# Performance work log

Measured on AMD Instinct MI355X. Metric: run time of the kernel, lower is better.

Reference implementation:

```python
import jax, jax.numpy as jnp
import numpy as np

N = 100000
E = 1600000
F_IN = 512
HEADS = 8
C1 = 8          # per-head channels layer 1
C2 = 16         # num_classes, layer 2 (heads=1)
NEG_SLOPE = 0.2


def gat_conv(x, W, att_src, att_dst, bias, edge_index, heads, ch):
    """PyG-style GATConv (eval mode, add_self_loops=True, concat).
    x: [N, Fin], W: [Fin, heads*ch], att_*: [heads, ch], bias: [heads*ch]."""
    n = x.shape[0]
    loop = jnp.arange(n, dtype=edge_index.dtype)
    src = jnp.concatenate([edge_index[0], loop])   # [E+N]
    dst = jnp.concatenate([edge_index[1], loop])

    h = (x @ W).reshape(n, heads, ch)                       # [N, H, C]
    a_src = jnp.einsum('nhc,hc->nh', h, att_src)            # [N, H]
    a_dst = jnp.einsum('nhc,hc->nh', h, att_dst)

    e = a_src[src] + a_dst[dst]                             # [E+N, H]
    e = jax.nn.leaky_relu(e, NEG_SLOPE)
    # segment softmax over destination nodes
    m = jax.ops.segment_max(e, dst, num_segments=n)         # [N, H]
    ex = jnp.exp(e - m[dst])
    denom = jax.ops.segment_sum(ex, dst, num_segments=n)    # [N, H]
    alpha = ex / (denom[dst] + 1e-16)                       # [E+N, H]

    msg = h[src] * alpha[..., None]                         # [E+N, H, C]
    out = jax.ops.segment_sum(msg, dst, num_segments=n)     # [N, H, C]
    return out.reshape(n, heads * ch) + bias


def setup_inputs() -> dict:
    key = jax.random.key(0)
    ks = jax.random.split(key, 10)
    glorot = lambda k, shape: jax.random.normal(k, shape, jnp.float32) * np.sqrt(2.0 / (shape[0] + shape[-1]))
    return {
        'x': jax.random.normal(ks[0], (N, F_IN), jnp.float32),
        'edge_index': jax.random.randint(ks[1], (2, E), 0, N, jnp.int64),
        'W1': glorot(ks[2], (F_IN, HEADS * C1)),
        'att_src1': glorot(ks[3], (HEADS, C1)),
        'att_dst1': glorot(ks[4], (HEADS, C1)),
        'b1': jnp.zeros((HEADS * C1,), jnp.float32),
        'W2': glorot(ks[5], (HEADS * C1, C2)),
        'att_src2': glorot(ks[6], (1, C2)),
        'att_dst2': glorot(ks[7], (1, C2)),
        'b2': jnp.zeros((C2,), jnp.float32),
    }


def reference(x, edge_index, W1, att_src1, att_dst1, b1, W2, att_src2, att_dst2, b2):
    # eval mode: all F.dropout / internal attention dropout are identity
    h = gat_conv(x, W1, att_src1, att_dst1, b1, edge_index, HEADS, C1)   # [N, 64]
    h = jax.nn.elu(h)
    h = gat_conv(h, W2, att_src2, att_dst2, b2, edge_index, 1, C2)       # [N, C2]
    return jax.nn.log_softmax(h, axis=1)
```

## Files before the change

### kernel.cpp

```cpp
#include <hip/hip_runtime.h>
#include <hip/hip_bf16.h>

#define NEG_SLOPE 0.2f

typedef __attribute__((ext_vector_type(8))) short  bf16x8;
typedef __attribute__((ext_vector_type(8))) unsigned short u16x8;
typedef __attribute__((ext_vector_type(4))) unsigned short u16x4;
typedef __attribute__((ext_vector_type(4))) float  f32x4;

static __device__ __forceinline__ ushort f2bf(float f) {
    union { float f; unsigned int u; } c; c.f = f;
    unsigned int r = c.u + 0x7fffu + ((c.u >> 16) & 1u);
    return (ushort)(r >> 16);
}
static __device__ __forceinline__ float bf2f(ushort u) {
    union { unsigned int u; float f; } c; c.u = ((unsigned int)u) << 16;
    return c.f;
}

__global__ __launch_bounds__(256) void gemm1_mfma(
    const float* __restrict__ x, const float* __restrict__ W,
    const float* __restrict__ att_src, const float* __restrict__ att_dst,
    ushort* __restrict__ h1b, float* __restrict__ asrc, float* __restrict__ adst, int n)
{
    __shared__ ushort Bs[64][520];
    const int t    = threadIdx.x;
    const int lane = t & 63;
    const int wv   = t >> 6;
    const int rb   = blockIdx.x * 64;
    const int m    = lane & 15;
    const int kg   = lane >> 4;

    #pragma unroll 4
    for (int i = 0; i < 32; ++i) {
        int idx = (t + i * 256) * 4;
        float4 v = *(const float4*)(W + idx);
        int k = idx >> 6, c = idx & 63;
        Bs[c + 0][k] = f2bf(v.x); Bs[c + 1][k] = f2bf(v.y);
        Bs[c + 2][k] = f2bf(v.z); Bs[c + 3][k] = f2bf(v.w);
    }

    const int arow  = rb + wv * 16 + m;
    const int arowc = min(arow, n - 1);
    const float* xp = x + (size_t)arowc * 512 + kg * 8;

    f32x4 acc[4] = {};
    __syncthreads();

    #pragma unroll 8
    for (int k32 = 0; k32 < 16; ++k32) {
        float4 lo = *(const float4*)(xp + k32 * 32);
        float4 hi = *(const float4*)(xp + k32 * 32 + 4);
        u16x8 a;
        a[0] = f2bf(lo.x); a[1] = f2bf(lo.y); a[2] = f2bf(lo.z); a[3] = f2bf(lo.w);
        a[4] = f2bf(hi.x); a[5] = f2bf(hi.y); a[6] = f2bf(hi.z); a[7] = f2bf(hi.w);
        bf16x8 af = *(bf16x8*)&a;
        #pragma unroll
        for (int t4 = 0; t4 < 4; ++t4) {
            bf16x8 bfr = *(const bf16x8*)&Bs[t4 * 16 + m][k32 * 32 + kg * 8];
            acc[t4] = __builtin_amdgcn_mfma_f32_16x16x32_bf16(af, bfr, acc[t4], 0, 0, 0);
        }
    }

    #pragma unroll
    for (int t4 = 0; t4 < 4; ++t4) {
        const float as_w = att_src[t4 * 16 + m];
        const float ad_w = att_dst[t4 * 16 + m];
        #pragma unroll
        for (int i = 0; i < 4; ++i) {
            int gr = rb + wv * 16 + kg * 4 + i;
            float v = acc[t4][i];
            float ps = v * as_w, pd = v * ad_w;
            ps += __shfl_xor(ps, 1); pd += __shfl_xor(pd, 1);
            ps += __shfl_xor(ps, 2); pd += __shfl_xor(pd, 2);
            ps += __shfl_xor(ps, 4); pd += __shfl_xor(pd, 4);
            if (gr < n) {
                h1b[(size_t)gr * 64 + t4 * 16 + m] = f2bf(v);
                if ((m & 7) == 0) {
                    int h = t4 * 2 + (m >> 3);
                    asrc[gr * 8 + h] = ps;
                    adst[gr * 8 + h] = pd;
                }
            }
        }
    }
}

__global__ __launch_bounds__(256) void hist_k(
    const int* __restrict__ ei, int* __restrict__ cnt, int* __restrict__ slot, int E)
{
    int t = blockIdx.x * blockDim.x + threadIdx.x;
    if (t < E) slot[t] = atomicAdd(&cnt[ei[E + t]], 1);
}

#define SCAN_B 256
#define SCAN_T 256

__global__ __launch_bounds__(SCAN_T) void scan_a(const int* __restrict__ cnt, int* __restrict__ bsum, int n)
{
    __shared__ int sh[SCAN_T];
    const int tid = threadIdx.x;
    const int per = (n + SCAN_B * SCAN_T - 1) / (SCAN_B * SCAN_T);
    const int lo = (blockIdx.x * SCAN_T + tid) * per;
    const int hi = min(n, lo + per);
    int s = 0;
    for (int i = lo; i < hi; ++i) s += cnt[i];
    sh[tid] = s;
    __syncthreads();
    #pragma unroll
    for (int o = SCAN_T / 2; o; o >>= 1) {
        if (tid < o) sh[tid] += sh[tid + o];
        __syncthreads();
    }
    if (tid == 0) bsum[blockIdx.x] = sh[0];
}

__global__ __launch_bounds__(SCAN_T) void scan_b(
    const int* __restrict__ cnt, const int* __restrict__ bsum,
    int* __restrict__ rowptr, int n, int E)
{
    __shared__ int sb[SCAN_B];
    __shared__ int sh[SCAN_T];
    const int tid = threadIdx.x;
    sb[tid] = bsum[tid];
    __syncthreads();
    #pragma unroll
    for (int o = 1; o < SCAN_B; o <<= 1) {
        int v = (tid >= o) ? sb[tid - o] : 0;
        __syncthreads();
        sb[tid] += v;
        __syncthreads();
    }
    const int boff = (blockIdx.x == 0) ? 0 : sb[blockIdx.x - 1];

    const int per = (n + SCAN_B * SCAN_T - 1) / (SCAN_B * SCAN_T);
    const int lo = (blockIdx.x * SCAN_T + tid) * per;
    const int hi = min(n, lo + per);
    int s = 0;
    for (int i = lo; i < hi; ++i) s += cnt[i];
    sh[tid] = s;
    __syncthreads();
    #pragma unroll
    for (int o = 1; o < SCAN_T; o <<= 1) {
        int v = (tid >= o) ? sh[tid - o] : 0;
        __syncthreads();
        sh[tid] += v;
        __syncthreads();
    }
    int excl = boff + ((tid == 0) ? 0 : sh[tid - 1]);
    for (int i = lo; i < hi; ++i) { rowptr[i] = excl; excl += cnt[i]; }
    if (blockIdx.x == 0 && tid == 0) rowptr[n] = E;
}

__global__ __launch_bounds__(256) void scatter_k(
    const int* __restrict__ ei, const int* __restrict__ rowptr,
    const int* __restrict__ slot, int* __restrict__ ssrc, int E)
{
    int t = blockIdx.x * blockDim.x + threadIdx.x;
    if (t >= E) return;
    int d = ei[E + t];
    ssrc[rowptr[d] + slot[t]] = ei[t];
}

__global__ __launch_bounds__(256) void agg1_k(
    const int* __restrict__ rowptr, const int* __restrict__ ssrc,
    const float* __restrict__ asrc1, const float* __restrict__ adst1,
    const ushort* __restrict__ h1b, const float* __restrict__ b1,
    const float* __restrict__ W2, const float* __restrict__ att_src2, const float* __restrict__ att_dst2,
    ushort* __restrict__ h2b, float* __restrict__ asrc2, float* __restrict__ adst2, int n)
{
    __shared__ float Ws2[64 * 17];
    __shared__ float sv[4][64];
    const int t = threadIdx.x;
    #pragma unroll
    for (int k = 0; k < 4; ++k) {
        int idx = t + k * 256;
        Ws2[(idx >> 4) * 17 + (idx & 15)] = W2[idx];
    }
    __syncthreads();

    const int wv = t >> 6;
    const int j  = t & 63;
    const int g  = j >> 3;
    const int h  = j & 7;
    const int node = blockIdx.x * 4 + wv;
    const bool active = node < n;

    if (active) {
        const int d = node;
        const int start = rowptr[d], end = rowptr[d + 1];
        const float adsth = adst1[d * 8 + h];
        float acc0[8] = {}, acc1[8] = {};
        float dsum0 = 0.f, dsum1 = 0.f;
        for (int base = start - 1; base < end; base += 16) {
            int i0 = base + g;
            int i1 = i0 + 8;
            if (i0 < end) {
                int s = (i0 < start) ? d : ssrc[i0];
                float e = asrc1[s * 8 + h] + adsth;
                e = e > 0.f ? e : NEG_SLOPE * e;
                float ex = __expf(e);
                dsum0 += ex;
                u16x8 hv = *(const u16x8*)(h1b + (size_t)s * 64 + h * 8);
                #pragma unroll
                for (int c = 0; c < 8; ++c) acc0[c] += ex * bf2f(hv[c]);
            }
            if (i1 < end) {
                int s = ssrc[i1];
                float e = asrc1[s * 8 + h] + adsth;
                e = e > 0.f ? e : NEG_SLOPE * e;
                float ex = __expf(e);
                dsum1 += ex;
                u16x8 hv = *(const u16x8*)(h1b + (size_t)s * 64 + h * 8);
                #pragma unroll
                for (int c = 0; c < 8; ++c) acc1[c] += ex * bf2f(hv[c]);
            }
        }
        float dsum = dsum0 + dsum1;
        float acc[8];
        #pragma unroll
        for (int c = 0; c < 8; ++c) acc[c] = acc0[c] + acc1[c];
        #pragma unroll
        for (int o = 8; o < 64; o <<= 1) {
            dsum += __shfl_xor(dsum, o);
            #pragma unroll
            for (int c = 0; c < 8; ++c) acc[c] += __shfl_xor(acc[c], o);
        }
        if (g == 0) {
            float den = dsum + 1e-16f;
            #pragma unroll
            for (int c = 0; c < 8; ++c) {
                float v = acc[c] / den + b1[h * 8 + c];
                v = v > 0.f ? v : (__expf(v) - 1.f);
                sv[wv][h * 8 + c] = v;
            }
        }
    }
    __syncthreads();

    if (active) {
        const int c = j & 15, q = j >> 4;
        float p = 0.f;
        #pragma unroll
        for (int r = 0; r < 16; ++r)
            p += sv[wv][q * 16 + r] * Ws2[(q * 16 + r) * 17 + c];
        p += __shfl_xor(p, 16);
        p += __shfl_xor(p, 32);
        if (j < 16) h2b[(size_t)node * 16 + j] = f2bf(p);
        float as2 = p * att_src2[c];
        float ad2 = p * att_dst2[c];
        #pragma unroll
        for (int o = 1; o < 16; o <<= 1) { as2 += __shfl_xor(as2, o, 16); ad2 += __shfl_xor(ad2, o, 16); }
        if (j == 0) { asrc2[node] = as2; adst2[node] = ad2; }
    }
}

__global__ __launch_bounds__(256) void agg2_k(
    const int* __restrict__ rowptr, const int* __restrict__ ssrc,
    const float* __restrict__ asrc2, const float* __restrict__ adst2,
    const ushort* __restrict__ h2b, const float* __restrict__ b2,
    float* __restrict__ out, int n)
{
    const int t = threadIdx.x;
    const int node = blockIdx.x * 4 + (t >> 6);
    if (node >= n) return;
    const int j = t & 63;
    const int g = j >> 2;
    const int q = j & 3;
    const int d = node;
    const int start = rowptr[d], end = rowptr[d + 1];
    const float adst_d = adst2[d];

    float acc0[4] = {}, acc1[4] = {};
    float dsum0 = 0.f, dsum1 = 0.f;
    for (int base = start - 1; base < end; base += 32) {
        int i0 = base + g;
        int i1 = i0 + 16;
        if (i0 < end) {
            int s = (i0 < start) ? d : ssrc[i0];
            float e = asrc2[s] + adst_d;
            e = e > 0.f ? e : NEG_SLOPE * e;
            float ex = __expf(e);
            dsum0 += ex;
            u16x4 hv = *(const u16x4*)(h2b + (size_t)s * 16 + q * 4);
            #pragma unroll
            for (int c = 0; c < 4; ++c) acc0[c] += ex * bf2f(hv[c]);
        }
        if (i1 < end) {
            int s = ssrc[i1];
            float e = asrc2[s] + adst_d;
            e = e > 0.f ? e : NEG_SLOPE * e;
            float ex = __expf(e);
            dsum1 += ex;
            u16x4 hv = *(const u16x4*)(h2b + (size_t)s * 16 + q * 4);
            #pragma unroll
            for (int c = 0; c < 4; ++c) acc1[c] += ex * bf2f(hv[c]);
        }
    }
    float dsum = dsum0 + dsum1;
    float acc[4];
    #pragma unroll
    for (int c = 0; c < 4; ++c) acc[c] = acc0[c] + acc1[c];
    #pragma unroll
    for (int o = 4; o < 64; o <<= 1) {
        dsum += __shfl_xor(dsum, o);
        #pragma unroll
        for (int c = 0; c < 4; ++c) acc[c] += __shfl_xor(acc[c], o);
    }

    const float den = dsum + 1e-16f;
    float v[4];
    float m = -1e30f;
    #pragma unroll
    for (int c = 0; c < 4; ++c) {
        v[c] = acc[c] / den + b2[q * 4 + c];
        m = fmaxf(m, v[c]);
    }
    m = fmaxf(m, __shfl_xor(m, 1));
    m = fmaxf(m, __shfl_xor(m, 2));
    float s2 = 0.f;
    #pragma unroll
    for (int c = 0; c < 4; ++c) s2 += __expf(v[c] - m);
    s2 += __shfl_xor(s2, 1);
    s2 += __shfl_xor(s2, 2);
    const float lse = m + logf(s2);
    if (j < 4) {
        float4 o4 = make_float4(v[0] - lse, v[1] - lse, v[2] - lse, v[3] - lse);
        *(float4*)(out + (size_t)d * 16 + q * 4) = o4;
    }
}

extern "C" void kernel_launch(void* const* d_in, const int* in_sizes, int n_in,
                              void* d_out, int out_size, void* d_ws, size_t ws_size,
                              hipStream_t stream) {
    const float* x        = (const float*)d_in[0];
    const int*   ei       = (const int*)d_in[1];
    const float* W1       = (const float*)d_in[2];
    const float* att_src1 = (const float*)d_in[3];
    const float* att_dst1 = (const float*)d_in[4];
    const float* b1       = (const float*)d_in[5];
    const float* W2       = (const float*)d_in[6];
    const float* att_src2 = (const float*)d_in[7];
    const float* att_dst2 = (const float*)d_in[8];
    const float* b2       = (const float*)d_in[9];
    float* out = (float*)d_out;

    const int n = in_sizes[0] / 512;
    const int E = in_sizes[1] / 2;

    char* base = (char*)d_ws;
    ushort* h1b   = (ushort*)(base);
    ushort* h2b   = (ushort*)(base + (size_t)128 * n);
    float*  asrc1 = (float*) (base + (size_t)160 * n);
    float*  adst1 = (float*) (base + (size_t)192 * n);
    float*  asrc2 = (float*) (base + (size_t)224 * n);
    float*  adst2 = (float*) (base + (size_t)228 * n);
    int*    rowptr= (int*)   (base + (size_t)232 * n);
    int*    cnt   = (int*)   (base + (size_t)236 * n + 4);
    int*    bsum  = (int*)   (base + (size_t)240 * n + 4);
    int*    slot  = (int*)   (base + (size_t)240 * n + 4 + 1024);
    int*    ssrc  = slot + E;

    hipMemsetAsync(cnt, 0, (size_t)4 * n, stream);

    hist_k<<<(E + 255) / 256, 256, 0, stream>>>(ei, cnt, slot, E);
    scan_a<<<SCAN_B, SCAN_T, 0, stream>>>(cnt, bsum, n);
    scan_b<<<SCAN_B, SCAN_T, 0, stream>>>(cnt, bsum, rowptr, n, E);
    scatter_k<<<(E + 255) / 256, 256, 0, stream>>>(ei, rowptr, slot, ssrc, E);

    gemm1_mfma<<<(n + 63) / 64, 256, 0, stream>>>(x, W1, att_src1, att_dst1, h1b, asrc1, adst1, n);

    agg1_k<<<(n + 3) / 4, 256, 0, stream>>>(rowptr, ssrc, asrc1, adst1, h1b, b1,
                                            W2, att_src2, att_dst2, h2b, asrc2, adst2, n);

    agg2_k<<<(n + 3) / 4, 256, 0, stream>>>(rowptr, ssrc, asrc2, adst2, h2b, b2, out, n);
}
```

Before: 300.2 us.

## Pre-transpose W1 to bf16, double-buffer x loads, and use 128-row gemm1 blocks

A new small kernel converts W1 to a transposed bf16 copy once per call, so each gemm1 block loads B into shared memory with plain vector copies instead of per-block conversion and scattered stores. gemm1 now uses 512 threads covering 128 rows, which halves how many times each block loads W. The x row loads are prefetched two k-steps ahead to hide global-memory latency behind the MFMAs. The trade-off is an extra launch, plus higher register use and lower occupancy from the larger blocks. The workspace layout is also recomputed with aligned offsets.

```diff
diff --git a/kernel.cpp b/kernel.cpp
--- a/kernel.cpp
+++ b/kernel.cpp
@@ -18,8 +18,16 @@
     return c.f;
 }
 
-__global__ __launch_bounds__(256) void gemm1_mfma(
-    const float* __restrict__ x, const float* __restrict__ W,
+__global__ __launch_bounds__(256) void prep_w1(const float* __restrict__ W, ushort* __restrict__ W1T)
+{
+    int idx = blockIdx.x * 256 + threadIdx.x;
+    if (idx >= 64 * 512) return;
+    int c = idx >> 9, k = idx & 511;
+    W1T[idx] = f2bf(W[k * 64 + c]);
+}
+
+__global__ __launch_bounds__(512, 4) void gemm1_mfma(
+    const float* __restrict__ x, const ushort* __restrict__ W1T,
     const float* __restrict__ att_src, const float* __restrict__ att_dst,
     ushort* __restrict__ h1b, float* __restrict__ asrc, float* __restrict__ adst, int n)
 {
@@ -27,17 +35,16 @@
     const int t    = threadIdx.x;
     const int lane = t & 63;
     const int wv   = t >> 6;
-    const int rb   = blockIdx.x * 64;
+    const int rb   = blockIdx.x * 128;
     const int m    = lane & 15;
     const int kg   = lane >> 4;
 
-    #pragma unroll 4
-    for (int i = 0; i < 32; ++i) {
-        int idx = (t + i * 256) * 4;
-        float4 v = *(const float4*)(W + idx);
-        int k = idx >> 6, c = idx & 63;
-        Bs[c + 0][k] = f2bf(v.x); Bs[c + 1][k] = f2bf(v.y);
-        Bs[c + 2][k] = f2bf(v.z); Bs[c + 3][k] = f2bf(v.w);
+    #pragma unroll
+    for (int i = 0; i < 8; ++i) {
+        int chunk = t + i * 512;
+        int c  = chunk >> 6;
+        int ko = (chunk & 63) * 8;
+        *(u16x8*)&Bs[c][ko] = *(const u16x8*)(W1T + c * 512 + ko);
     }
 
     const int arow  = rb + wv * 16 + m;
@@ -47,19 +54,27 @@
     f32x4 acc[4] = {};
     __syncthreads();
 
-    #pragma unroll 8
+    float4 lo0 = *(const float4*)(xp);
+    float4 hi0 = *(const float4*)(xp + 4);
+    float4 lo1 = *(const float4*)(xp + 32);
+    float4 hi1 = *(const float4*)(xp + 36);
+    #pragma unroll
     for (int k32 = 0; k32 < 16; ++k32) {
-        float4 lo = *(const float4*)(xp + k32 * 32);
-        float4 hi = *(const float4*)(xp + k32 * 32 + 4);
+        float4 nlo = {}, nhi = {};
+        if (k32 < 14) {
+            nlo = *(const float4*)(xp + (k32 + 2) * 32);
+            nhi = *(const float4*)(xp + (k32 + 2) * 32 + 4);
+        }
         u16x8 a;
-        a[0] = f2bf(lo.x); a[1] = f2bf(lo.y); a[2] = f2bf(lo.z); a[3] = f2bf(lo.w);
-        a[4] = f2bf(hi.x); a[5] = f2bf(hi.y); a[6] = f2bf(hi.z); a[7] = f2bf(hi.w);
+        a[0] = f2bf(lo0.x); a[1] = f2bf(lo0.y); a[2] = f2bf(lo0.z); a[3] = f2bf(lo0.w);
+        a[4] = f2bf(hi0.x); a[5] = f2bf(hi0.y); a[6] = f2bf(hi0.z); a[7] = f2bf(hi0.w);
         bf16x8 af = *(bf16x8*)&a;
         #pragma unroll
         for (int t4 = 0; t4 < 4; ++t4) {
             bf16x8 bfr = *(const bf16x8*)&Bs[t4 * 16 + m][k32 * 32 + kg * 8];
             acc[t4] = __builtin_amdgcn_mfma_f32_16x16x32_bf16(af, bfr, acc[t4], 0, 0, 0);
         }
+        lo0 = lo1; hi0 = hi1; lo1 = nlo; hi1 = nhi;
     }
 
     #pragma unroll
@@ -330,6 +345,8 @@
     }
 }
 
+static inline size_t align_up(size_t v, size_t a) { return (v + a - 1) & ~(a - 1); }
+
 extern "C" void kernel_launch(void* const* d_in, const int* in_sizes, int n_in,
                               void* d_out, int out_size, void* d_ws, size_t ws_size,
                               hipStream_t stream) {
@@ -349,26 +366,30 @@
     const int E = in_sizes[1] / 2;
 
     char* base = (char*)d_ws;
-    ushort* h1b   = (ushort*)(base);
-    ushort* h2b   = (ushort*)(base + (size_t)128 * n);
-    float*  asrc1 = (float*) (base + (size_t)160 * n);
-    float*  adst1 = (float*) (base + (size_t)192 * n);
-    float*  asrc2 = (float*) (base + (size_t)224 * n);
-    float*  adst2 = (float*) (base + (size_t)228 * n);
-    int*    rowptr= (int*)   (base + (size_t)232 * n);
-    int*    cnt   = (int*)   (base + (size_t)236 * n + 4);
-    int*    bsum  = (int*)   (base + (size_t)240 * n + 4);
-    int*    slot  = (int*)   (base + (size_t)240 * n + 4 + 1024);
-    int*    ssrc  = slot + E;
+    size_t off = 0;
+    ushort* h1b   = (ushort*)(base + off); off = align_up(off + (size_t)128 * n, 64);
+    ushort* h2b   = (ushort*)(base + off); off = align_up(off + (size_t)32 * n, 64);
+    float*  asrc1 = (float*) (base + off); off = align_up(off + (size_t)32 * n, 64);
+    float*  adst1 = (float*) (base + off); off = align_up(off + (size_t)32 * n, 64);
+    float*  asrc2 = (float*) (base + off); off = align_up(off + (size_t)4 * n, 64);
+    float*  adst2 = (float*) (base + off); off = align_up(off + (size_t)4 * n, 64);
+    ushort* W1T   = (ushort*)(base + off); off = align_up(off + (size_t)65536, 64);
+    int*    rowptr= (int*)   (base + off); off = align_up(off + (size_t)4 * (n + 1), 64);
+    int*    cnt   = (int*)   (base + off); off = align_up(off + (size_t)4 * n, 64);
+    int*    bsum  = (int*)   (base + off); off = align_up(off + (size_t)1024, 64);
+    int*    slot  = (int*)   (base + off); off = align_up(off + (size_t)4 * E, 64);
+    int*    ssrc  = (int*)   (base + off);
 
     hipMemsetAsync(cnt, 0, (size_t)4 * n, stream);
+
+    prep_w1<<<128, 256, 0, stream>>>(W1, W1T);
 
     hist_k<<<(E + 255) / 256, 256, 0, stream>>>(ei, cnt, slot, E);
     scan_a<<<SCAN_B, SCAN_T, 0, stream>>>(cnt, bsum, n);
     scan_b<<<SCAN_B, SCAN_T, 0, stream>>>(cnt, bsum, rowptr, n, E);
     scatter_k<<<(E + 255) / 256, 256, 0, stream>>>(ei, rowptr, slot, ssrc, E);
 
-    gemm1_mfma<<<(n + 63) / 64, 256, 0, stream>>>(x, W1, att_src1, att_dst1, h1b, asrc1, adst1, n);
+    gemm1_mfma<<<(n + 127) / 128, 512, 0, stream>>>(x, W1T, att_src1, att_dst1, h1b, asrc1, adst1, n);
 
     agg1_k<<<(n + 3) / 4, 256, 0, stream>>>(rowptr, ssrc, asrc1, adst1, h1b, b1,
                                             W2, att_src2, att_dst2, h2b, asrc2, adst2, n);
```

After: 269.3 us. -10.3%, faster.
